# Optimization experiments

Measured on AMD Instinct MI355X. Metric: run time of the kernel, lower is better.

Reference implementation:

```python
import jax, jax.numpy as jnp
import numpy as np

N_NODES = 100000


def setup_inputs() -> dict:
    key = jax.random.key(0)
    k1, k2, k3, k4, k5 = jax.random.split(key, 5)
    features = jax.random.normal(k1, (N_NODES, 512), dtype=jnp.float32)
    edge_src = jax.random.randint(k2, (640000,), 0, N_NODES, dtype=jnp.int64)
    edge_dst = jax.random.randint(k3, (640000,), 0, N_NODES, dtype=jnp.int64)
    edge_weight = jax.random.uniform(k4, (640000,), dtype=jnp.float32)
    weights = jax.random.normal(k5, (512, 128), dtype=jnp.float32) * (2.0 / 512) ** 0.5  # kaiming-ish scale
    bias = jnp.zeros((128,), dtype=jnp.float32)
    return {
        "features": features,
        "edge_src": edge_src,
        "edge_dst": edge_dst,
        "edge_weight": edge_weight,
        "weights": weights,
        "bias": bias,
    }


def reference(features, edge_src, edge_dst, edge_weight, weights, bias):
    # X' = A @ (X @ W) + b, with sparse A given as COO edges (src -> dst).
    h = jnp.matmul(features, weights)                      # [N, d_out] dense GEMM
    msg = edge_weight[:, None] * h[edge_src]               # [E, d_out] gather + scale
    out = jax.ops.segment_sum(msg, edge_dst, num_segments=N_NODES)  # sparse aggregation
    return out + bias
```

## Files before the change

### kernel.cpp

```cpp
#include <hip/hip_runtime.h>


#define D_IN  512
#define D_OUT 128
#define CAP   32

typedef __attribute__((ext_vector_type(8))) short short8;
typedef __attribute__((ext_vector_type(4))) float f32x4;
typedef __attribute__((ext_vector_type(4))) int i32x4;
typedef __attribute__((ext_vector_type(8))) unsigned short u16x8;
typedef __attribute__((ext_vector_type(2))) unsigned long long u64x2;

static __device__ __forceinline__ unsigned short f2bf(float f) {
    unsigned u = __float_as_uint(f);
    unsigned r = (u + 0x7FFFu + ((u >> 16) & 1u)) >> 16;
    return (unsigned short)r;
}

static __device__ __forceinline__ int pack2(float lo, float hi) {
    return (int)((__float_as_uint(hi) & 0xFFFF0000u) | (__float_as_uint(lo) >> 16));
}

__global__ __launch_bounds__(256) void prep_kernel(const float* __restrict__ W,
                                                   unsigned short* __restrict__ Wt,
                                                   int* __restrict__ deg, int M) {
    int t = blockIdx.x * 256 + threadIdx.x;
    if (t < D_OUT * D_IN) {
        int n = t >> 9;
        int k = t & 511;
        Wt[t] = f2bf(W[(size_t)k * D_OUT + n]);
    }
    if (t < M) deg[t] = 0;
}

__global__ __launch_bounds__(256, 3) void gemm_build_kernel(
        const float* __restrict__ X, const unsigned short* __restrict__ Wt,
        unsigned short* __restrict__ H, int M,
        const int* __restrict__ src, const int* __restrict__ dst,
        const float* __restrict__ w, int* __restrict__ deg,
        unsigned long long* __restrict__ bucket, int E, int nG) {
    if ((int)blockIdx.x >= nG) {
        int e = ((int)blockIdx.x - nG) * 256 + threadIdx.x;
        if (e < E) {
            int d = dst[e];
            int pos = atomicAdd(&deg[d], 1);
            if (pos < CAP)
                bucket[(size_t)d * CAP + pos] =
                    ((unsigned long long)__float_as_uint(w[e]) << 32) | (unsigned)src[e];
        }
        return;
    }

    const int tid = threadIdx.x;
    const int lane = tid & 63;
    const int wv = tid >> 6;
    const int block_row = blockIdx.x * 128;

    const int m = lane & 15;
    const int q = lane >> 4;
    const int wave_row = wv * 32;

    const float* Xr[2];
#pragma unroll
    for (int rg = 0; rg < 2; rg++) {
        int grow = block_row + wave_row + rg * 16 + m;
        if (grow >= M) grow = M - 1;
        Xr[rg] = X + (size_t)grow * D_IN;
    }
    const unsigned short* Wn[8];
#pragma unroll
    for (int cg = 0; cg < 8; cg++) Wn[cg] = Wt + (size_t)(cg * 16 + m) * D_IN;

    f32x4 acc[2][8];
#pragma unroll
    for (int a = 0; a < 2; a++)
#pragma unroll
        for (int b = 0; b < 8; b++) acc[a][b] = (f32x4){0.f, 0.f, 0.f, 0.f};

#pragma unroll 4
    for (int ks = 0; ks < 16; ks++) {
        const int kb = ks * 32 + q * 8;
        short8 afr[2];
#pragma unroll
        for (int rg = 0; rg < 2; rg++) {
            f32x4 u0 = *reinterpret_cast<const f32x4*>(Xr[rg] + kb);
            f32x4 u1 = *reinterpret_cast<const f32x4*>(Xr[rg] + kb + 4);
            i32x4 ai;
            ai.x = pack2(u0.x, u0.y);
            ai.y = pack2(u0.z, u0.w);
            ai.z = pack2(u1.x, u1.y);
            ai.w = pack2(u1.z, u1.w);
            afr[rg] = __builtin_bit_cast(short8, ai);
        }
        short8 bfr[8];
#pragma unroll
        for (int cg = 0; cg < 8; cg++)
            bfr[cg] = *reinterpret_cast<const short8*>(Wn[cg] + kb);
#pragma unroll
        for (int rg = 0; rg < 2; rg++)
#pragma unroll
            for (int cg = 0; cg < 8; cg++)
                acc[rg][cg] = __builtin_amdgcn_mfma_f32_16x16x32_bf16(
                    afr[rg], bfr[cg], acc[rg][cg], 0, 0, 0);
    }

#pragma unroll
    for (int rg = 0; rg < 2; rg++) {
#pragma unroll
        for (int r = 0; r < 4; r++) {
            int grow = block_row + wave_row + rg * 16 + q * 4 + r;
            if (grow < M) {
#pragma unroll
                for (int cg = 0; cg < 8; cg++)
                    H[(size_t)grow * D_OUT + cg * 16 + m] = f2bf(acc[rg][cg][r]);
            }
        }
    }
}

__global__ __launch_bounds__(256) void agg_kernel(const unsigned short* __restrict__ H,
                                                  const int* __restrict__ deg,
                                                  const unsigned long long* __restrict__ bucket,
                                                  const float* __restrict__ bias,
                                                  float* __restrict__ out, int M) {
    int row = blockIdx.x * 16 + (threadIdx.x >> 4);
    if (row >= M) return;
    int sub = threadIdx.x & 15;

    f32x4 b0 = *reinterpret_cast<const f32x4*>(bias + sub * 8);
    f32x4 b1 = *reinterpret_cast<const f32x4*>(bias + sub * 8 + 4);
    float acc[8] = {b0.x, b0.y, b0.z, b0.w, b1.x, b1.y, b1.z, b1.w};

    int n = deg[row];
    if (n > CAP) n = CAP;
    const unsigned long long* bp = bucket + (size_t)row * CAP;

    int j = 0;
    for (; j + 4 <= n; j += 4) {
        u64x2 q0 = __builtin_nontemporal_load(reinterpret_cast<const u64x2*>(bp + j));
        u64x2 q1 = __builtin_nontemporal_load(reinterpret_cast<const u64x2*>(bp + j + 2));
        unsigned long long p0 = q0[0];
        unsigned long long p1 = q0[1];
        unsigned long long p2 = q1[0];
        unsigned long long p3 = q1[1];
        u16x8 v0 = *reinterpret_cast<const u16x8*>(
            H + (size_t)(unsigned)(p0 & 0xFFFFFFFFull) * D_OUT + sub * 8);
        u16x8 v1 = *reinterpret_cast<const u16x8*>(
            H + (size_t)(unsigned)(p1 & 0xFFFFFFFFull) * D_OUT + sub * 8);
        u16x8 v2 = *reinterpret_cast<const u16x8*>(
            H + (size_t)(unsigned)(p2 & 0xFFFFFFFFull) * D_OUT + sub * 8);
        u16x8 v3 = *reinterpret_cast<const u16x8*>(
            H + (size_t)(unsigned)(p3 & 0xFFFFFFFFull) * D_OUT + sub * 8);
        float w0 = __uint_as_float((unsigned)(p0 >> 32));
        float w1 = __uint_as_float((unsigned)(p1 >> 32));
        float w2 = __uint_as_float((unsigned)(p2 >> 32));
        float w3 = __uint_as_float((unsigned)(p3 >> 32));
#pragma unroll
        for (int c = 0; c < 8; c++) {
            acc[c] += w0 * __uint_as_float((unsigned)v0[c] << 16);
            acc[c] += w1 * __uint_as_float((unsigned)v1[c] << 16);
            acc[c] += w2 * __uint_as_float((unsigned)v2[c] << 16);
            acc[c] += w3 * __uint_as_float((unsigned)v3[c] << 16);
        }
    }
    for (; j < n; j++) {
        unsigned long long p0 = bp[j];
        float w0 = __uint_as_float((unsigned)(p0 >> 32));
        u16x8 v0 = *reinterpret_cast<const u16x8*>(
            H + (size_t)(unsigned)(p0 & 0xFFFFFFFFull) * D_OUT + sub * 8);
#pragma unroll
        for (int c = 0; c < 8; c++)
            acc[c] += w0 * __uint_as_float((unsigned)v0[c] << 16);
    }

    f32x4 o0 = {acc[0], acc[1], acc[2], acc[3]};
    f32x4 o1 = {acc[4], acc[5], acc[6], acc[7]};
    __builtin_nontemporal_store(o0, reinterpret_cast<f32x4*>(out + (size_t)row * D_OUT + sub * 8));
    __builtin_nontemporal_store(o1, reinterpret_cast<f32x4*>(out + (size_t)row * D_OUT + sub * 8 + 4));
}

extern "C" void kernel_launch(void* const* d_in, const int* in_sizes, int n_in,
                              void* d_out, int out_size, void* d_ws, size_t ws_size,
                              hipStream_t stream) {
    const float* features    = (const float*)d_in[0];
    const int*   edge_src    = (const int*)d_in[1];
    const int*   edge_dst    = (const int*)d_in[2];
    const float* edge_weight = (const float*)d_in[3];
    const float* weights     = (const float*)d_in[4];
    const float* bias        = (const float*)d_in[5];
    float* out = (float*)d_out;

    const int M = in_sizes[0] / D_IN;
    const int E = in_sizes[1];

    char* ws = (char*)d_ws;
    unsigned short* hbf = (unsigned short*)(ws);
    unsigned short* Wt  = (unsigned short*)(ws + 25600000);
    int* deg            = (int*)(ws + 25731072);
    unsigned long long* bucket = (unsigned long long*)(ws + 26131456);

    int mx = (M > D_OUT * D_IN) ? M : (D_OUT * D_IN);
    prep_kernel<<<(mx + 255) / 256, 256, 0, stream>>>(weights, Wt, deg, M);

    const int nG = (M + 127) / 128;
    const int nB = (E + 255) / 256;
    gemm_build_kernel<<<nG + nB, 256, 0, stream>>>(features, Wt, hbf, M,
                                                   edge_src, edge_dst, edge_weight,
                                                   deg, bucket, E, nG);

    agg_kernel<<<(M + 15) / 16, 256, 0, stream>>>(hbf, deg, bucket, bias, out, M);
}
```

Measured before the change: 401.7 us.

## Software-pipeline GEMM loads and pad aggregation buckets with zeroed entries

The GEMM loop now prefetches A fragments three k-steps ahead and B fragments two steps ahead into register buffers, with the loop fully unrolled and occupancy lowered to 2 blocks per CU to make room for the extra registers. The prep kernel zero-fills the whole bucket array so the aggregation loop can always process entries in groups of four, with no scalar tail, since padded entries carry zero weight. This hides global load latency in the GEMM and removes tail divergence in aggregation. The cost is writing the full 25.6MB bucket array every call, plus higher register pressure and lower occupancy in the GEMM.

```diff
diff --git a/kernel.cpp b/kernel.cpp
--- a/kernel.cpp
+++ b/kernel.cpp
@@ -23,7 +23,9 @@
 
 __global__ __launch_bounds__(256) void prep_kernel(const float* __restrict__ W,
                                                    unsigned short* __restrict__ Wt,
-                                                   int* __restrict__ deg, int M) {
+                                                   int* __restrict__ deg,
+                                                   unsigned long long* __restrict__ bucket,
+                                                   int M) {
     int t = blockIdx.x * 256 + threadIdx.x;
     if (t < D_OUT * D_IN) {
         int n = t >> 9;
@@ -31,9 +33,14 @@
         Wt[t] = f2bf(W[(size_t)k * D_OUT + n]);
     }
     if (t < M) deg[t] = 0;
-}
-
-__global__ __launch_bounds__(256, 3) void gemm_build_kernel(
+    const int stride = gridDim.x * 256;
+    const int npair = M * (CAP / 2);
+    u64x2 z = {0ull, 0ull};
+    for (int i = t; i < npair; i += stride)
+        __builtin_nontemporal_store(z, reinterpret_cast<u64x2*>(bucket) + i);
+}
+
+__global__ __launch_bounds__(256, 2) void gemm_build_kernel(
         const float* __restrict__ X, const unsigned short* __restrict__ Wt,
         unsigned short* __restrict__ H, int M,
         const int* __restrict__ src, const int* __restrict__ dst,
@@ -77,14 +84,38 @@
 #pragma unroll
         for (int b = 0; b < 8; b++) acc[a][b] = (f32x4){0.f, 0.f, 0.f, 0.f};
 
-#pragma unroll 4
+    f32x4 Ab[3][2][2];
+    short8 Bb[2][8];
+
+#define KB(ks) ((ks) * 32 + q * 8)
+#define LOAD_A(st, ks)                                                         \
+    do {                                                                       \
+        _Pragma("unroll") for (int rg = 0; rg < 2; rg++) {                     \
+            Ab[st][rg][0] = *reinterpret_cast<const f32x4*>(Xr[rg] + KB(ks));  \
+            Ab[st][rg][1] = *reinterpret_cast<const f32x4*>(Xr[rg] + KB(ks) + 4); \
+        }                                                                      \
+    } while (0)
+#define LOAD_B(st, ks)                                                         \
+    do {                                                                       \
+        _Pragma("unroll") for (int cg = 0; cg < 8; cg++)                       \
+            Bb[st][cg] = *reinterpret_cast<const short8*>(Wn[cg] + KB(ks));    \
+    } while (0)
+
+    LOAD_A(0, 0);
+    LOAD_A(1, 1);
+    LOAD_A(2, 2);
+    LOAD_B(0, 0);
+    LOAD_B(1, 1);
+
+#pragma unroll
     for (int ks = 0; ks < 16; ks++) {
-        const int kb = ks * 32 + q * 8;
+        const int sA = ks % 3;
+        const int sB = ks % 2;
         short8 afr[2];
 #pragma unroll
         for (int rg = 0; rg < 2; rg++) {
-            f32x4 u0 = *reinterpret_cast<const f32x4*>(Xr[rg] + kb);
-            f32x4 u1 = *reinterpret_cast<const f32x4*>(Xr[rg] + kb + 4);
+            f32x4 u0 = Ab[sA][rg][0];
+            f32x4 u1 = Ab[sA][rg][1];
             i32x4 ai;
             ai.x = pack2(u0.x, u0.y);
             ai.y = pack2(u0.z, u0.w);
@@ -92,17 +123,18 @@
             ai.w = pack2(u1.z, u1.w);
             afr[rg] = __builtin_bit_cast(short8, ai);
         }
-        short8 bfr[8];
-#pragma unroll
-        for (int cg = 0; cg < 8; cg++)
-            bfr[cg] = *reinterpret_cast<const short8*>(Wn[cg] + kb);
+        if (ks + 3 < 16) LOAD_A(sA, ks + 3);
 #pragma unroll
         for (int rg = 0; rg < 2; rg++)
 #pragma unroll
             for (int cg = 0; cg < 8; cg++)
                 acc[rg][cg] = __builtin_amdgcn_mfma_f32_16x16x32_bf16(
-                    afr[rg], bfr[cg], acc[rg][cg], 0, 0, 0);
-    }
+                    afr[rg], Bb[sB][cg], acc[rg][cg], 0, 0, 0);
+        if (ks + 2 < 16) LOAD_B(sB, ks + 2);
+    }
+#undef KB
+#undef LOAD_A
+#undef LOAD_B
 
 #pragma unroll
     for (int rg = 0; rg < 2; rg++) {
@@ -135,8 +167,7 @@
     if (n > CAP) n = CAP;
     const unsigned long long* bp = bucket + (size_t)row * CAP;
 
-    int j = 0;
-    for (; j + 4 <= n; j += 4) {
+    for (int j = 0; j < n; j += 4) {
         u64x2 q0 = __builtin_nontemporal_load(reinterpret_cast<const u64x2*>(bp + j));
         u64x2 q1 = __builtin_nontemporal_load(reinterpret_cast<const u64x2*>(bp + j + 2));
         unsigned long long p0 = q0[0];
@@ -163,15 +194,6 @@
             acc[c] += w3 * __uint_as_float((unsigned)v3[c] << 16);
         }
     }
-    for (; j < n; j++) {
-        unsigned long long p0 = bp[j];
-        float w0 = __uint_as_float((unsigned)(p0 >> 32));
-        u16x8 v0 = *reinterpret_cast<const u16x8*>(
-            H + (size_t)(unsigned)(p0 & 0xFFFFFFFFull) * D_OUT + sub * 8);
-#pragma unroll
-        for (int c = 0; c < 8; c++)
-            acc[c] += w0 * __uint_as_float((unsigned)v0[c] << 16);
-    }
 
     f32x4 o0 = {acc[0], acc[1], acc[2], acc[3]};
     f32x4 o1 = {acc[4], acc[5], acc[6], acc[7]};
@@ -200,7 +222,7 @@
     unsigned long long* bucket = (unsigned long long*)(ws + 26131456);
 
     int mx = (M > D_OUT * D_IN) ? M : (D_OUT * D_IN);
-    prep_kernel<<<(mx + 255) / 256, 256, 0, stream>>>(weights, Wt, deg, M);
+    prep_kernel<<<(mx + 255) / 256, 256, 0, stream>>>(weights, Wt, deg, bucket, M);
 
     const int nG = (M + 127) / 128;
     const int nB = (E + 255) / 256;
```

Measured after the change: 411.7 us. 2.5% more time.
